# Kernel optimization log

Hardware: AMD Instinct MI355X
Metric: run time of the kernel (lower is better)

## Reference

```python
import jax, jax.numpy as jnp
import numpy as np

N_NODES = 100000
N_EDGES = 3200000
EMBED_DIM = 64
BATCH = 16384


def setup_inputs() -> dict:
    key = jax.random.key(0)
    k1, k2, k3, k4 = jax.random.split(key, 4)
    gcn_weight = jax.random.normal(k1, (N_NODES, EMBED_DIM), dtype=jnp.float32) * 0.1
    gcn_bias = jnp.zeros((EMBED_DIM,), dtype=jnp.float32)
    linear_weight = jax.random.normal(k2, (N_NODES, 1), dtype=jnp.float32) * 0.1
    linear_bias = jnp.zeros((1,), dtype=jnp.float32)
    edge_index = jax.random.randint(k3, (2, N_EDGES), 0, N_NODES, dtype=jnp.int64)
    interaction_pairs = jax.random.randint(k4, (BATCH, 2), 0, N_NODES, dtype=jnp.int64)
    return {
        "gcn_weight": gcn_weight,
        "gcn_bias": gcn_bias,
        "linear_weight": linear_weight,
        "linear_bias": linear_bias,
        "edge_index": edge_index,
        "interaction_pairs": interaction_pairs,
    }


def _gcn_conv_identity_features(gcn_weight, gcn_bias, edge_index):
    # Features X = I, so X @ W = W. GCNConv output = D^{-1/2}(A+I)D^{-1/2} W + b.
    src, dst = edge_index[0], edge_index[1]
    ones = jnp.ones((src.shape[0],), dtype=gcn_weight.dtype)
    # degree (with self loop) computed on destination nodes, as in PyG gcn_norm
    deg = jax.ops.segment_sum(ones, dst, num_segments=N_NODES) + 1.0
    dinv = jax.lax.rsqrt(deg)  # [N]
    norm = dinv[src] * dinv[dst]  # [E]
    msg = gcn_weight[src] * norm[:, None]  # [E, D] -- dominant memory traffic
    agg = jax.ops.segment_sum(msg, dst, num_segments=N_NODES)  # [N, D]
    # self-loop term: norm_ii = 1/deg[i]
    out = agg + gcn_weight * (dinv * dinv)[:, None] + gcn_bias
    return out


def reference(gcn_weight, gcn_bias, linear_weight, linear_bias, edge_index, interaction_pairs):
    node_emb = _gcn_conv_identity_features(gcn_weight, gcn_bias, edge_index)  # [N, D]
    e = node_emb[interaction_pairs]  # [B, 2, D] gather
    # FM pairwise interaction: 0.5 * sum_d ((sum_f e)^2 - sum_f e^2)
    sum_sq = jnp.square(jnp.sum(e, axis=1))  # [B, D]
    sq_sum = jnp.sum(jnp.square(e), axis=1)  # [B, D]
    fm = 0.5 * jnp.sum(sum_sq - sq_sum, axis=1, keepdims=True)  # [B, 1]
    # FeaturesLinear: sum of per-node scalar embeddings + bias
    lin = jnp.sum(linear_weight[interaction_pairs], axis=1) + linear_bias  # [B, 1]
    return jnp.squeeze(lin + fm, axis=1)  # [B]
```

## Files before the change

kernel.cpp:

```cpp
#include <hip/hip_runtime.h>

#define N_NODES 100000
#define N_EDGES 3200000
#define BATCH 16384
#define MAX_SLOTS 32768

#define NW 12500
#define SLICES 256
#define EPS2 12500
#define I4PS2 3125

#define NBUCK 256
#define BSH 7

#define OFF_SLOT      0
#define OFF_DINV      400064
#define OFF_NODELIST  800064
#define OFF_BTOT      931136
#define OFF_BPART     932160
#define OFF_SLOTSTART 1194304
#define OFF_PARTIALS  1325440
#define OFF_WH        14125440
#define OFF_BINS      26925440
#define OFF_BINS2     31725440
#define OFF_EMB       36525440

__device__ __forceinline__ unsigned bfr(float f) {
    unsigned u = __float_as_uint(f);
    return (u + 0x7FFFu + ((u >> 16) & 1u)) >> 16;
}
__device__ __forceinline__ float bfx(unsigned h) {
    return __uint_as_float(h << 16);
}

__global__ void k_flags(const int* __restrict__ pairs, unsigned* __restrict__ slot,
                        int* __restrict__ nodelist) {
    int i = blockIdx.x * blockDim.x + threadIdx.x;
    if (i < 2 * BATCH) {
        int n = pairs[i];
        nodelist[i] = n;
        slot[n] = (unsigned)(i + 1);
    }
}

__device__ __forceinline__ int cert(int d, const unsigned* __restrict__ slot,
                                    const int* __restrict__ nodelist) {
    unsigned r = slot[d];
    unsigned idx = r - 1u;
    if (idx < (unsigned)MAX_SLOTS && nodelist[idx] == d) return (int)idx;
    return -1;
}

__global__ void k_hist(const int* __restrict__ dst, const unsigned* __restrict__ slot,
                       const int* __restrict__ nodelist,
                       unsigned* __restrict__ partials, int* __restrict__ bpart) {
    __shared__ unsigned h[NW];
    __shared__ int lc[NBUCK];
    int g = blockIdx.x;
    for (int i = threadIdx.x; i < NW; i += 512) h[i] = 0;
    if (threadIdx.x < NBUCK) lc[threadIdx.x] = 0;
    __syncthreads();
    const int4* d4 = (const int4*)(dst + g * EPS2);
    for (int i = threadIdx.x; i < I4PS2; i += 512) {
        int4 v = d4[i];
        atomicAdd(&h[v.x >> 3], 1u << ((v.x & 7) << 2));
        atomicAdd(&h[v.y >> 3], 1u << ((v.y & 7) << 2));
        atomicAdd(&h[v.z >> 3], 1u << ((v.z & 7) << 2));
        atomicAdd(&h[v.w >> 3], 1u << ((v.w & 7) << 2));
        int t;
        t = cert(v.x, slot, nodelist); if (t >= 0) atomicAdd(&lc[t >> BSH], 1);
        t = cert(v.y, slot, nodelist); if (t >= 0) atomicAdd(&lc[t >> BSH], 1);
        t = cert(v.z, slot, nodelist); if (t >= 0) atomicAdd(&lc[t >> BSH], 1);
        t = cert(v.w, slot, nodelist); if (t >= 0) atomicAdd(&lc[t >> BSH], 1);
    }
    __syncthreads();
    unsigned* outp = partials + (unsigned)g * NW;
    for (int i = threadIdx.x; i < NW; i += 512) outp[i] = h[i];
    if (threadIdx.x < NBUCK) bpart[threadIdx.x * SLICES + g] = lc[threadIdx.x];
}

__global__ void k_mid(const unsigned* __restrict__ partials, const float4* __restrict__ w4,
                      float* __restrict__ dinv, uint4* __restrict__ wh4,
                      int* __restrict__ bpart, int* __restrict__ btot) {
    if (blockIdx.x >= 391) {
        __shared__ int t[SLICES];
        int b = blockIdx.x - 391, g = threadIdx.x;
        int v = bpart[b * SLICES + g];
        t[g] = v;
        __syncthreads();
        for (int off = 1; off < SLICES; off <<= 1) {
            int x = (g >= off) ? t[g - off] : 0;
            __syncthreads();
            t[g] += x;
            __syncthreads();
        }
        bpart[b * SLICES + g] = t[g] - v;
        if (g == SLICES - 1) btot[b] = t[g];
        return;
    }
    __shared__ unsigned pA[256], pB[256], pC[256], pD[256];
    __shared__ float sdinv[256];
    int blk = blockIdx.x;
    int wi = threadIdx.x & 31, sg = threadIdx.x >> 5;
    int w = blk * 32 + wi;
    unsigned A = 0, B = 0, C = 0, D = 0;
    if (w < NW) {
        const unsigned* q = partials + w;
#pragma unroll
        for (int ch = 0; ch < 2; ++ch) {
            unsigned x = 0, y = 0;
#pragma unroll
            for (int k = 0; k < 16; ++k) {
                unsigned v = q[(unsigned)(sg * 32 + ch * 16 + k) * NW];
                x += v & 0x0F0F0F0Fu;
                y += (v >> 4) & 0x0F0F0F0Fu;
            }
            A += x & 0x00FF00FFu;
            B += (x >> 8) & 0x00FF00FFu;
            C += y & 0x00FF00FFu;
            D += (y >> 8) & 0x00FF00FFu;
        }
    }
    pA[threadIdx.x] = A; pB[threadIdx.x] = B; pC[threadIdx.x] = C; pD[threadIdx.x] = D;
    __syncthreads();
    if (threadIdx.x < 32 && w < NW) {
        unsigned sA = 0, sB = 0, sC = 0, sD = 0;
#pragma unroll
        for (int k = 0; k < 8; ++k) {
            sA += pA[k * 32 + wi]; sB += pB[k * 32 + wi];
            sC += pC[k * 32 + wi]; sD += pD[k * 32 + wi];
        }
        float4 d0, d1;
        d0.x = rsqrtf((float)(sA & 0xFFFFu) + 1.0f);
        d0.y = rsqrtf((float)(sC & 0xFFFFu) + 1.0f);
        d0.z = rsqrtf((float)(sB & 0xFFFFu) + 1.0f);
        d0.w = rsqrtf((float)(sD & 0xFFFFu) + 1.0f);
        d1.x = rsqrtf((float)(sA >> 16) + 1.0f);
        d1.y = rsqrtf((float)(sC >> 16) + 1.0f);
        d1.z = rsqrtf((float)(sB >> 16) + 1.0f);
        d1.w = rsqrtf((float)(sD >> 16) + 1.0f);
        ((float4*)dinv)[w * 2] = d0;
        ((float4*)dinv)[w * 2 + 1] = d1;
        int lb = wi * 8;
        sdinv[lb + 0] = d0.x; sdinv[lb + 1] = d0.y; sdinv[lb + 2] = d0.z; sdinv[lb + 3] = d0.w;
        sdinv[lb + 4] = d1.x; sdinv[lb + 5] = d1.y; sdinv[lb + 6] = d1.z; sdinv[lb + 7] = d1.w;
    }
    __syncthreads();
#pragma unroll
    for (int it = 0; it < 8; ++it) {
        int k = blk * 2048 + it * 256 + threadIdx.x;
        if (k < N_NODES * 8) {
            float4 va = w4[k * 2];
            float4 vb = w4[k * 2 + 1];
            float d = sdinv[(k >> 3) - blk * 256];
            uint4 o;
            o.x = bfr(va.x * d) | (bfr(va.y * d) << 16);
            o.y = bfr(va.z * d) | (bfr(va.w * d) << 16);
            o.z = bfr(vb.x * d) | (bfr(vb.y * d) << 16);
            o.w = bfr(vb.z * d) | (bfr(vb.w * d) << 16);
            wh4[k] = o;
        }
    }
}

__global__ void k_bscatter(const int* __restrict__ src, const int* __restrict__ dst,
                           const unsigned* __restrict__ slot, const int* __restrict__ nodelist,
                           const int* __restrict__ bpart, const int* __restrict__ btot,
                           int* __restrict__ bins) {
    __shared__ int tb[NBUCK], vv[NBUCK], cur[NBUCK];
    int g = blockIdx.x;
    int t = threadIdx.x;
    if (t < NBUCK) { int v = btot[t]; vv[t] = v; tb[t] = v; }
    __syncthreads();
    for (int off = 1; off < NBUCK; off <<= 1) {
        int x = (t < NBUCK && t >= off) ? tb[t - off] : 0;
        __syncthreads();
        if (t < NBUCK) tb[t] += x;
        __syncthreads();
    }
    if (t < NBUCK) cur[t] = tb[t] - vv[t] + bpart[t * SLICES + g];
    __syncthreads();
    const int4* d4 = (const int4*)(dst + g * EPS2);
    const int4* s4 = (const int4*)(src + g * EPS2);
    for (int i = t; i < I4PS2; i += 512) {
        int4 d = d4[i];
        int4 s = s4[i];
        int sl;
        sl = cert(d.x, slot, nodelist);
        if (sl >= 0) { int pos = atomicAdd(&cur[sl >> BSH], 1); bins[pos] = ((sl & 127) << 17) | s.x; }
        sl = cert(d.y, slot, nodelist);
        if (sl >= 0) { int pos = atomicAdd(&cur[sl >> BSH], 1); bins[pos] = ((sl & 127) << 17) | s.y; }
        sl = cert(d.z, slot, nodelist);
        if (sl >= 0) { int pos = atomicAdd(&cur[sl >> BSH], 1); bins[pos] = ((sl & 127) << 17) | s.z; }
        sl = cert(d.w, slot, nodelist);
        if (sl >= 0) { int pos = atomicAdd(&cur[sl >> BSH], 1); bins[pos] = ((sl & 127) << 17) | s.w; }
    }
}

__global__ void k_bsort(const int* __restrict__ btot, const int* __restrict__ bins,
                        int* __restrict__ slotstart, int* __restrict__ bins2) {
    __shared__ int tb[NBUCK], vv[NBUCK];
    __shared__ int lc[128], st[128];
    int b = blockIdx.x;
    int tid = threadIdx.x;
    { int v = btot[tid]; vv[tid] = v; tb[tid] = v; }
    __syncthreads();
    for (int off = 1; off < NBUCK; off <<= 1) {
        int x = (tid >= off) ? tb[tid - off] : 0;
        __syncthreads();
        tb[tid] += x;
        __syncthreads();
    }
    int beg = tb[b] - vv[b];
    int end = beg + vv[b];
    if (tid < 128) lc[tid] = 0;
    __syncthreads();
    for (int j = beg + tid; j < end; j += 256)
        atomicAdd(&lc[(bins[j] >> 17) & 127], 1);
    __syncthreads();
    if (tid < 128) st[tid] = lc[tid];
    __syncthreads();
    for (int off = 1; off < 128; off <<= 1) {
        int v = (tid < 128 && tid >= off) ? st[tid - off] : 0;
        __syncthreads();
        if (tid < 128) st[tid] += v;
        __syncthreads();
    }
    if (tid < 128) {
        int s0 = beg + st[tid] - lc[tid];
        slotstart[(b << 7) + tid] = s0;
        lc[tid] = s0;
    }
    if (b == NBUCK - 1 && tid == 0) slotstart[MAX_SLOTS] = tb[NBUCK - 1];
    __syncthreads();
    for (int j = beg + tid; j < end; j += 256) {
        int e = bins[j];
        int pos = atomicAdd(&lc[(e >> 17) & 127], 1);
        bins2[pos] = e & 0x1FFFF;
    }
}

__global__ void k_gather(const int* __restrict__ nodelist, const int* __restrict__ slotstart,
                         const int* __restrict__ bins2, const uint4* __restrict__ wh4,
                         const float* __restrict__ dinv, const float4* __restrict__ bias4,
                         uint4* __restrict__ emb4) {
    int s = (blockIdx.x * blockDim.x + threadIdx.x) >> 6;
    int lane = threadIdx.x & 63;
    int rg = lane >> 3, dp = lane & 7;
    int beg = slotstart[s], end = slotstart[s + 1];
    float a0 = 0.f, a1 = 0.f, a2 = 0.f, a3 = 0.f, a4 = 0.f, a5 = 0.f, a6 = 0.f, a7 = 0.f;
    int j = beg;
    for (; j + 16 <= end; j += 16) {
        int e0 = bins2[j + rg];
        int e1 = bins2[j + 8 + rg];
        uint4 oa = wh4[(e0 << 3) + dp];
        uint4 ob = wh4[(e1 << 3) + dp];
        a0 += bfx(oa.x) + bfx(ob.x);
        a1 += bfx(oa.x >> 16) + bfx(ob.x >> 16);
        a2 += bfx(oa.y) + bfx(ob.y);
        a3 += bfx(oa.y >> 16) + bfx(ob.y >> 16);
        a4 += bfx(oa.z) + bfx(ob.z);
        a5 += bfx(oa.z >> 16) + bfx(ob.z >> 16);
        a6 += bfx(oa.w) + bfx(ob.w);
        a7 += bfx(oa.w >> 16) + bfx(ob.w >> 16);
    }
    for (; j < end; j += 8) {
        if (rg < end - j) {
            int e0 = bins2[j + rg];
            uint4 oa = wh4[(e0 << 3) + dp];
            a0 += bfx(oa.x); a1 += bfx(oa.x >> 16);
            a2 += bfx(oa.y); a3 += bfx(oa.y >> 16);
            a4 += bfx(oa.z); a5 += bfx(oa.z >> 16);
            a6 += bfx(oa.w); a7 += bfx(oa.w >> 16);
        }
    }
#pragma unroll
    for (int m = 8; m <= 32; m <<= 1) {
        a0 += __shfl_xor(a0, m, 64); a1 += __shfl_xor(a1, m, 64);
        a2 += __shfl_xor(a2, m, 64); a3 += __shfl_xor(a3, m, 64);
        a4 += __shfl_xor(a4, m, 64); a5 += __shfl_xor(a5, m, 64);
        a6 += __shfl_xor(a6, m, 64); a7 += __shfl_xor(a7, m, 64);
    }
    if (rg == 0) {
        int n = nodelist[s];
        float dn = dinv[n];
        uint4 u = wh4[(n << 3) + dp];
        float4 b0 = bias4[dp * 2], b1 = bias4[dp * 2 + 1];
        float r0 = (a0 + bfx(u.x)) * dn + b0.x;
        float r1 = (a1 + bfx(u.x >> 16)) * dn + b0.y;
        float r2 = (a2 + bfx(u.y)) * dn + b0.z;
        float r3 = (a3 + bfx(u.y >> 16)) * dn + b0.w;
        float r4 = (a4 + bfx(u.z)) * dn + b1.x;
        float r5 = (a5 + bfx(u.z >> 16)) * dn + b1.y;
        float r6 = (a6 + bfx(u.w)) * dn + b1.z;
        float r7 = (a7 + bfx(u.w >> 16)) * dn + b1.w;
        uint4 o;
        o.x = bfr(r0) | (bfr(r1) << 16);
        o.y = bfr(r2) | (bfr(r3) << 16);
        o.z = bfr(r4) | (bfr(r5) << 16);
        o.w = bfr(r6) | (bfr(r7) << 16);
        emb4[(s << 3) + dp] = o;
    }
}

__global__ void k_final(const int* __restrict__ pairs, const unsigned* __restrict__ slot,
                        const uint2* __restrict__ emb2, const float* __restrict__ lw,
                        const float* __restrict__ lb, float* __restrict__ out) {
    int p = (blockIdx.x * blockDim.x + threadIdx.x) >> 4;
    int li = threadIdx.x & 15;
    if (p >= BATCH) return;
    int a = pairs[p * 2], b = pairs[p * 2 + 1];
    int sa = (int)slot[a] - 1;
    int sb = (int)slot[b] - 1;
    uint2 ua = emb2[(sa << 4) + li];
    uint2 ub = emb2[(sb << 4) + li];
    float prod = bfx(ua.x) * bfx(ub.x) + bfx(ua.x >> 16) * bfx(ub.x >> 16)
               + bfx(ua.y) * bfx(ub.y) + bfx(ua.y >> 16) * bfx(ub.y >> 16);
#pragma unroll
    for (int m = 1; m <= 8; m <<= 1) prod += __shfl_xor(prod, m, 64);
    if (li == 0) out[p] = lw[a] + lw[b] + lb[0] + prod;
}

extern "C" void kernel_launch(void* const* d_in, const int* in_sizes, int n_in,
                              void* d_out, int out_size, void* d_ws, size_t ws_size,
                              hipStream_t stream) {
    const float* gcn_weight    = (const float*)d_in[0];
    const float* gcn_bias      = (const float*)d_in[1];
    const float* linear_weight = (const float*)d_in[2];
    const float* linear_bias   = (const float*)d_in[3];
    const int*   edge_index    = (const int*)d_in[4];
    const int*   pairs         = (const int*)d_in[5];
    float* out = (float*)d_out;

    char* ws = (char*)d_ws;
    unsigned* slot      = (unsigned*)(ws + OFF_SLOT);
    float*    dinv      = (float*)   (ws + OFF_DINV);
    int*      nodelist  = (int*)     (ws + OFF_NODELIST);
    int*      btot      = (int*)     (ws + OFF_BTOT);
    int*      bpart     = (int*)     (ws + OFF_BPART);
    int*      slotstart = (int*)     (ws + OFF_SLOTSTART);
    unsigned* partials  = (unsigned*)(ws + OFF_PARTIALS);
    uint4*    wh4       = (uint4*)   (ws + OFF_WH);
    int*      bins      = (int*)     (ws + OFF_BINS);
    int*      bins2     = (int*)     (ws + OFF_BINS2);
    uint4*    emb4      = (uint4*)   (ws + OFF_EMB);
    uint2*    emb2      = (uint2*)   (ws + OFF_EMB);

    const int* src_arr = edge_index;
    const int* dst_arr = edge_index + N_EDGES;

    k_flags<<<128, 256, 0, stream>>>(pairs, slot, nodelist);
    k_hist<<<SLICES, 512, 0, stream>>>(dst_arr, slot, nodelist, partials, bpart);
    k_mid<<<391 + 256, 256, 0, stream>>>(partials, (const float4*)gcn_weight, dinv, wh4,
                                         bpart, btot);
    k_bscatter<<<SLICES, 512, 0, stream>>>(src_arr, dst_arr, slot, nodelist, bpart, btot, bins);
    k_bsort<<<NBUCK, 256, 0, stream>>>(btot, bins, slotstart, bins2);
    k_gather<<<MAX_SLOTS / 4, 256, 0, stream>>>(nodelist, slotstart, bins2, wh4,
                                                dinv, (const float4*)gcn_bias, emb4);
    k_final<<<1024, 256, 0, stream>>>(pairs, slot, emb2, linear_weight, linear_bias, out);
}
```

Measured before the change: 191.7 us.

## Fold flag setup into histogram and replace bucket prefix scan with atomic cursors

```diff
diff --git a/kernel.cpp b/kernel.cpp
--- a/kernel.cpp
+++ b/kernel.cpp
@@ -12,18 +12,18 @@
 
 #define NBUCK 256
 #define BSH 7
+#define BCAP 6144
 
 #define OFF_SLOT      0
-#define OFF_DINV      400064
-#define OFF_NODELIST  800064
-#define OFF_BTOT      931136
-#define OFF_BPART     932160
-#define OFF_SLOTSTART 1194304
-#define OFF_PARTIALS  1325440
-#define OFF_WH        14125440
-#define OFF_BINS      26925440
-#define OFF_BINS2     31725440
-#define OFF_EMB       36525440
+#define OFF_CURSOR    400000
+#define OFF_DINV      401024
+#define OFF_NODELIST  801024
+#define OFF_SLOTSTART 932096
+#define OFF_PARTIALS  1063232
+#define OFF_WH        13863232
+#define OFF_BINS      26663232
+#define OFF_BINS2     32954688
+#define OFF_EMB       37754688
 
 __device__ __forceinline__ unsigned bfr(float f) {
     unsigned u = __float_as_uint(f);
@@ -31,16 +31,6 @@
 }
 __device__ __forceinline__ float bfx(unsigned h) {
     return __uint_as_float(h << 16);
-}
-
-__global__ void k_flags(const int* __restrict__ pairs, unsigned* __restrict__ slot,
-                        int* __restrict__ nodelist) {
-    int i = blockIdx.x * blockDim.x + threadIdx.x;
-    if (i < 2 * BATCH) {
-        int n = pairs[i];
-        nodelist[i] = n;
-        slot[n] = (unsigned)(i + 1);
-    }
 }
 
 __device__ __forceinline__ int cert(int d, const unsigned* __restrict__ slot,
@@ -51,53 +41,38 @@
     return -1;
 }
 
-__global__ void k_hist(const int* __restrict__ dst, const unsigned* __restrict__ slot,
-                       const int* __restrict__ nodelist,
-                       unsigned* __restrict__ partials, int* __restrict__ bpart) {
+__global__ void k_hist(const int* __restrict__ dst, const int* __restrict__ pairs,
+                       unsigned* __restrict__ slot, int* __restrict__ nodelist,
+                       int* __restrict__ cursor, unsigned* __restrict__ partials) {
     __shared__ unsigned h[NW];
-    __shared__ int lc[NBUCK];
     int g = blockIdx.x;
-    for (int i = threadIdx.x; i < NW; i += 512) h[i] = 0;
-    if (threadIdx.x < NBUCK) lc[threadIdx.x] = 0;
+    int tid = threadIdx.x;
+    if (tid < 128) {
+        int fi = g * 128 + tid;
+        int n = pairs[fi];
+        nodelist[fi] = n;
+        slot[n] = (unsigned)(fi + 1);
+    } else if (g == 0 && tid < 384) {
+        int b = tid - 128;
+        cursor[b] = b * BCAP;
+    }
+    for (int i = tid; i < NW; i += 512) h[i] = 0;
     __syncthreads();
     const int4* d4 = (const int4*)(dst + g * EPS2);
-    for (int i = threadIdx.x; i < I4PS2; i += 512) {
+    for (int i = tid; i < I4PS2; i += 512) {
         int4 v = d4[i];
         atomicAdd(&h[v.x >> 3], 1u << ((v.x & 7) << 2));
         atomicAdd(&h[v.y >> 3], 1u << ((v.y & 7) << 2));
         atomicAdd(&h[v.z >> 3], 1u << ((v.z & 7) << 2));
         atomicAdd(&h[v.w >> 3], 1u << ((v.w & 7) << 2));
-        int t;
-        t = cert(v.x, slot, nodelist); if (t >= 0) atomicAdd(&lc[t >> BSH], 1);
-        t = cert(v.y, slot, nodelist); if (t >= 0) atomicAdd(&lc[t >> BSH], 1);
-        t = cert(v.z, slot, nodelist); if (t >= 0) atomicAdd(&lc[t >> BSH], 1);
-        t = cert(v.w, slot, nodelist); if (t >= 0) atomicAdd(&lc[t >> BSH], 1);
     }
     __syncthreads();
     unsigned* outp = partials + (unsigned)g * NW;
-    for (int i = threadIdx.x; i < NW; i += 512) outp[i] = h[i];
-    if (threadIdx.x < NBUCK) bpart[threadIdx.x * SLICES + g] = lc[threadIdx.x];
+    for (int i = tid; i < NW; i += 512) outp[i] = h[i];
 }
 
 __global__ void k_mid(const unsigned* __restrict__ partials, const float4* __restrict__ w4,
-                      float* __restrict__ dinv, uint4* __restrict__ wh4,
-                      int* __restrict__ bpart, int* __restrict__ btot) {
-    if (blockIdx.x >= 391) {
-        __shared__ int t[SLICES];
-        int b = blockIdx.x - 391, g = threadIdx.x;
-        int v = bpart[b * SLICES + g];
-        t[g] = v;
-        __syncthreads();
-        for (int off = 1; off < SLICES; off <<= 1) {
-            int x = (g >= off) ? t[g - off] : 0;
-            __syncthreads();
-            t[g] += x;
-            __syncthreads();
-        }
-        bpart[b * SLICES + g] = t[g] - v;
-        if (g == SLICES - 1) btot[b] = t[g];
-        return;
-    }
+                      float* __restrict__ dinv, uint4* __restrict__ wh4) {
     __shared__ unsigned pA[256], pB[256], pC[256], pD[256];
     __shared__ float sdinv[256];
     int blk = blockIdx.x;
@@ -165,45 +140,50 @@
 
 __global__ void k_bscatter(const int* __restrict__ src, const int* __restrict__ dst,
                            const unsigned* __restrict__ slot, const int* __restrict__ nodelist,
-                           const int* __restrict__ bpart, const int* __restrict__ btot,
-                           int* __restrict__ bins) {
-    __shared__ int tb[NBUCK], vv[NBUCK], cur[NBUCK];
+                           int* __restrict__ cursor, int* __restrict__ bins) {
+    __shared__ int ecnt[NBUCK];
     int g = blockIdx.x;
-    int t = threadIdx.x;
-    if (t < NBUCK) { int v = btot[t]; vv[t] = v; tb[t] = v; }
-    __syncthreads();
-    for (int off = 1; off < NBUCK; off <<= 1) {
-        int x = (t < NBUCK && t >= off) ? tb[t - off] : 0;
-        __syncthreads();
-        if (t < NBUCK) tb[t] += x;
-        __syncthreads();
-    }
-    if (t < NBUCK) cur[t] = tb[t] - vv[t] + bpart[t * SLICES + g];
+    int tid = threadIdx.x;
+    if (tid < NBUCK) ecnt[tid] = 0;
     __syncthreads();
     const int4* d4 = (const int4*)(dst + g * EPS2);
     const int4* s4 = (const int4*)(src + g * EPS2);
-    for (int i = t; i < I4PS2; i += 512) {
+    for (int i = tid; i < I4PS2; i += 512) {
+        int4 d = d4[i];
+        int t;
+        t = cert(d.x, slot, nodelist); if (t >= 0) atomicAdd(&ecnt[t >> BSH], 1);
+        t = cert(d.y, slot, nodelist); if (t >= 0) atomicAdd(&ecnt[t >> BSH], 1);
+        t = cert(d.z, slot, nodelist); if (t >= 0) atomicAdd(&ecnt[t >> BSH], 1);
+        t = cert(d.w, slot, nodelist); if (t >= 0) atomicAdd(&ecnt[t >> BSH], 1);
+    }
+    __syncthreads();
+    if (tid < NBUCK) {
+        int c = ecnt[tid];
+        ecnt[tid] = (c > 0) ? atomicAdd(&cursor[tid], c) : 0;
+    }
+    __syncthreads();
+    for (int i = tid; i < I4PS2; i += 512) {
         int4 d = d4[i];
         int4 s = s4[i];
-        int sl;
-        sl = cert(d.x, slot, nodelist);
-        if (sl >= 0) { int pos = atomicAdd(&cur[sl >> BSH], 1); bins[pos] = ((sl & 127) << 17) | s.x; }
-        sl = cert(d.y, slot, nodelist);
-        if (sl >= 0) { int pos = atomicAdd(&cur[sl >> BSH], 1); bins[pos] = ((sl & 127) << 17) | s.y; }
-        sl = cert(d.z, slot, nodelist);
-        if (sl >= 0) { int pos = atomicAdd(&cur[sl >> BSH], 1); bins[pos] = ((sl & 127) << 17) | s.z; }
-        sl = cert(d.w, slot, nodelist);
-        if (sl >= 0) { int pos = atomicAdd(&cur[sl >> BSH], 1); bins[pos] = ((sl & 127) << 17) | s.w; }
-    }
-}
-
-__global__ void k_bsort(const int* __restrict__ btot, const int* __restrict__ bins,
+        int t;
+        t = cert(d.x, slot, nodelist);
+        if (t >= 0) { int pos = atomicAdd(&ecnt[t >> BSH], 1); bins[pos] = ((t & 127) << 17) | s.x; }
+        t = cert(d.y, slot, nodelist);
+        if (t >= 0) { int pos = atomicAdd(&ecnt[t >> BSH], 1); bins[pos] = ((t & 127) << 17) | s.y; }
+        t = cert(d.z, slot, nodelist);
+        if (t >= 0) { int pos = atomicAdd(&ecnt[t >> BSH], 1); bins[pos] = ((t & 127) << 17) | s.z; }
+        t = cert(d.w, slot, nodelist);
+        if (t >= 0) { int pos = atomicAdd(&ecnt[t >> BSH], 1); bins[pos] = ((t & 127) << 17) | s.w; }
+    }
+}
+
+__global__ void k_bsort(const int* __restrict__ cursor, const int* __restrict__ bins,
                         int* __restrict__ slotstart, int* __restrict__ bins2) {
     __shared__ int tb[NBUCK], vv[NBUCK];
     __shared__ int lc[128], st[128];
     int b = blockIdx.x;
     int tid = threadIdx.x;
-    { int v = btot[tid]; vv[tid] = v; tb[tid] = v; }
+    { int c = cursor[tid] - tid * BCAP; vv[tid] = c; tb[tid] = c; }
     __syncthreads();
     for (int off = 1; off < NBUCK; off <<= 1) {
         int x = (tid >= off) ? tb[tid - off] : 0;
@@ -211,12 +191,13 @@
         tb[tid] += x;
         __syncthreads();
     }
-    int beg = tb[b] - vv[b];
-    int end = beg + vv[b];
+    int obeg = tb[b] - vv[b];
+    int ibeg = b * BCAP;
+    int cnt = vv[b];
     if (tid < 128) lc[tid] = 0;
     __syncthreads();
-    for (int j = beg + tid; j < end; j += 256)
-        atomicAdd(&lc[(bins[j] >> 17) & 127], 1);
+    for (int j = tid; j < cnt; j += 256)
+        atomicAdd(&lc[(bins[ibeg + j] >> 17) & 127], 1);
     __syncthreads();
     if (tid < 128) st[tid] = lc[tid];
     __syncthreads();
@@ -227,14 +208,14 @@
         __syncthreads();
     }
     if (tid < 128) {
-        int s0 = beg + st[tid] - lc[tid];
+        int s0 = obeg + st[tid] - lc[tid];
         slotstart[(b << 7) + tid] = s0;
         lc[tid] = s0;
     }
     if (b == NBUCK - 1 && tid == 0) slotstart[MAX_SLOTS] = tb[NBUCK - 1];
     __syncthreads();
-    for (int j = beg + tid; j < end; j += 256) {
-        int e = bins[j];
+    for (int j = tid; j < cnt; j += 256) {
+        int e = bins[ibeg + j];
         int pos = atomicAdd(&lc[(e >> 17) & 127], 1);
         bins2[pos] = e & 0x1FFFF;
     }
@@ -334,10 +315,9 @@
 
     char* ws = (char*)d_ws;
     unsigned* slot      = (unsigned*)(ws + OFF_SLOT);
+    int*      cursor    = (int*)     (ws + OFF_CURSOR);
     float*    dinv      = (float*)   (ws + OFF_DINV);
     int*      nodelist  = (int*)     (ws + OFF_NODELIST);
-    int*      btot      = (int*)     (ws + OFF_BTOT);
-    int*      bpart     = (int*)     (ws + OFF_BPART);
     int*      slotstart = (int*)     (ws + OFF_SLOTSTART);
     unsigned* partials  = (unsigned*)(ws + OFF_PARTIALS);
     uint4*    wh4       = (uint4*)   (ws + OFF_WH);
@@ -349,12 +329,10 @@
     const int* src_arr = edge_index;
     const int* dst_arr = edge_index + N_EDGES;
 
-    k_flags<<<128, 256, 0, stream>>>(pairs, slot, nodelist);
-    k_hist<<<SLICES, 512, 0, stream>>>(dst_arr, slot, nodelist, partials, bpart);
-    k_mid<<<391 + 256, 256, 0, stream>>>(partials, (const float4*)gcn_weight, dinv, wh4,
-                                         bpart, btot);
-    k_bscatter<<<SLICES, 512, 0, stream>>>(src_arr, dst_arr, slot, nodelist, bpart, btot, bins);
-    k_bsort<<<NBUCK, 256, 0, stream>>>(btot, bins, slotstart, bins2);
+    k_hist<<<SLICES, 512, 0, stream>>>(dst_arr, pairs, slot, nodelist, cursor, partials);
+    k_mid<<<391, 256, 0, stream>>>(partials, (const float4*)gcn_weight, dinv, wh4);
+    k_bscatter<<<SLICES, 512, 0, stream>>>(src_arr, dst_arr, slot, nodelist, cursor, bins);
+    k_bsort<<<NBUCK, 256, 0, stream>>>(cursor, bins, slotstart, bins2);
     k_gather<<<MAX_SLOTS / 4, 256, 0, stream>>>(nodelist, slotstart, bins2, wh4,
                                                 dinv, (const float4*)gcn_bias, emb4);
     k_final<<<1024, 256, 0, stream>>>(pairs, slot, emb2, linear_weight, linear_bias, out);
```

Result: no change. 195.5 us (+2.0%).
